# Optimization experiments

Hardware: AMD Instinct MI355X
Metric: run time of the kernel (lower is better)

The kernel has to match this reference:

```python
import jax, jax.numpy as jnp
import numpy as np

G, K = 60, 13  # SO(3) group size, neighbors per group element


def _gather(x, nei):
    # x: [N, C, G] -> [N, C, G, K] via fixed neighbor indices (len G*K)
    return x[:, :, nei].reshape(x.shape[0], x.shape[1], G, K)


def _comb(x, nei, W, b):
    # gather-then-(1,K)-Conv2d == contraction over (channel, neighbor)
    d = _gather(x, nei)                                   # [N,C,G,K]
    return jnp.einsum('ncgk,ock->nog', d, W) + b[None, :, None]


def setup_inputs() -> dict:
    key = jax.random.key(0)
    ks = jax.random.split(key, 8)
    N = 512
    feats = jax.random.normal(ks[0], (N, 32, G), jnp.float32)
    nei = jax.random.randint(ks[1], (G * K,), 0, G, jnp.int32)

    def w(k, o, c):
        return jax.random.normal(k, (o, c, K), jnp.float32) * (1.0 / np.sqrt(c * K))

    return {
        'feats': feats, 'nei': nei,
        'W_in': w(ks[2], 256, 32), 'b_in': jnp.zeros((256,), jnp.float32),
        'W_r1': w(ks[3], 512, 256), 'b_r1': jnp.zeros((512,), jnp.float32),
        'W_r2': w(ks[4], 256, 512), 'b_r2': jnp.zeros((256,), jnp.float32),
        'W_out': w(ks[5], 32, 256), 'b_out': jnp.zeros((32,), jnp.float32),
    }


def reference(feats, nei, W_in, b_in, W_r1, b_r1, W_r2, b_r2, W_out, b_out):
    # Conv_in: gather + (1,13) conv, 32 -> 256
    h = _comb(feats, nei, W_in, b_in)                      # [N,256,G]
    # Residual_Comb_Conv(256, 512, 256)
    r = jax.nn.relu(_comb(h, nei, W_r1, b_r1))             # [N,512,G]
    h = h + _comb(r, nei, W_r2, b_r2)                      # [N,256,G]
    # Conv_out: gather + (1,13) conv, 256 -> 32, then outer residual
    feats_eqv = _comb(h, nei, W_out, b_out) + feats        # [N,32,G]
    feats_inv = jnp.mean(feats_eqv, axis=-1)               # [N,32]
    feats_eqv = feats_eqv / jnp.maximum(
        jnp.linalg.norm(feats_eqv, axis=1, keepdims=True), 1e-4)
    feats_inv = feats_inv / jnp.maximum(
        jnp.linalg.norm(feats_inv, axis=1, keepdims=True), 1e-4)
    return feats_inv, feats_eqv
```

## Files before the change

kernel.cpp:

```cpp
#include <hip/hip_runtime.h>
#include <stdint.h>

#define GSZ 60
#define KNB 13
#define NPT 512

typedef __attribute__((ext_vector_type(4))) float f32x4;
typedef __attribute__((ext_vector_type(8))) short s16x8;

__device__ __forceinline__ ushort f2bf(float f) {
  union { float f; unsigned u; } v; v.f = f;
  unsigned r = v.u + 0x7fffu + ((v.u >> 16) & 1u);
  return (ushort)(r >> 16);
}
__device__ __forceinline__ float bf2f(ushort h) {
  union { unsigned u; float f; } v; v.u = ((unsigned)h) << 16;
  return v.f;
}

__device__ __forceinline__ void gload_lds16(const void* gsrc, void* ldst) {
  __builtin_amdgcn_global_load_lds(
      (const __attribute__((address_space(1))) uint32_t*)gsrc,
      (__attribute__((address_space(3))) uint32_t*)ldst, 16, 0, 0);
}

template <int N>
__device__ __forceinline__ void vwaitN() {
  if constexpr (N == 0) asm volatile("s_waitcnt vmcnt(0)" ::: "memory");
  else if constexpr (N == 3) asm volatile("s_waitcnt vmcnt(3)" ::: "memory");
  else if constexpr (N == 4) asm volatile("s_waitcnt vmcnt(4)" ::: "memory");
  else if constexpr (N == 6) asm volatile("s_waitcnt vmcnt(6)" ::: "memory");
  else asm volatile("s_waitcnt vmcnt(8)" ::: "memory");
}

__global__ __launch_bounds__(256) void prep_feats_k(const float* __restrict__ feats,
                                                    ushort* __restrict__ X0) {
  int idx = blockIdx.x * 256 + threadIdx.x;
  if (idx >= 61 * NPT * 32) return;
  int c = idx & 31;
  int t = idx >> 5;
  int n = t % NPT;
  int g = t / NPT;
  X0[idx] = (g < GSZ) ? f2bf(feats[(n * 32 + c) * GSZ + g]) : (ushort)0;
}

__global__ __launch_bounds__(256) void prep_wb_k(const float* __restrict__ W,
                                                 ushort* __restrict__ Wb,
                                                 int O, int OPAD, int C, int KPAD) {
  int idx = blockIdx.x * 256 + threadIdx.x;
  if (idx >= OPAD * KPAD) return;
  int o = idx / KPAD;
  int kk = idx - o * KPAD;
  int k = kk / C;
  int c = kk - k * C;
  Wb[idx] = (o < O && k < KNB) ? f2bf(W[(o * C + c) * KNB + k]) : (ushort)0;
}

template <int CIN, int KTOT, int OPAD, int OREAL, int BN, int MODE, bool RELU>
__global__ __launch_bounds__(256) void comb_gemm(
    const ushort* __restrict__ Xin, const ushort* __restrict__ Wb,
    const float* __restrict__ bias, const int* __restrict__ nei,
    ushort* __restrict__ Xout, float* __restrict__ Eq,
    const float* __restrict__ feats, int qb, int qe) {
  constexpr int BM = 128;
  constexpr int BK = 64;
  constexpr int TO = OPAD / BN;
  constexpr int TN = NPT / BM;
  constexpr int WN = BN / 2;
  constexpr int N_REP = WN / 16;
  constexpr int M_REP = 4;
  constexpr int CSH = (CIN == 32) ? 5 : (CIN == 256) ? 8 : 9;
  static_assert(CIN == (1 << CSH), "CIN pow2");

  __shared__ ushort smA[2][BM * BK];
  __shared__ ushort smB[2][BN * BK];
  __shared__ int nei_sh[16];

  const int nwg = TO * TN * GSZ;
  const int cpx = nwg >> 3;
  const int bid = blockIdx.x;
  const int idx = (bid & 7) * cpx + (bid >> 3);
  const int g = idx / (TO * TN);
  const int rem = idx - g * (TO * TN);
  const int nt = rem / TO;
  const int ot = rem - nt * TO;
  const int n0 = nt * BM;
  const int o0 = ot * BN;

  const int t = threadIdx.x;
  if (t < 14) nei_sh[t] = (t < KNB) ? nei[g * KNB + t] : GSZ;
  __syncthreads();

  const int w = t >> 6;
  const int l = t & 63;
  const int lrow = l & 15;
  const int lkg = l >> 4;
  const int wr = w >> 1;
  const int wc = w & 1;
  const int srow_w = w * 8;
  const int sr = l >> 3;
  const int slot = l & 7;

  int laneA[BM / 32], laneB[BN / 32], swz[BM / 32];
#pragma unroll
  for (int j = 0; j < BM / 32; ++j) {
    const int r = j * 32 + srow_w + sr;
    swz[j] = (slot ^ (r & 7)) << 3;
    laneA[j] = ((n0 + r) << CSH) + swz[j];
  }
#pragma unroll
  for (int j = 0; j < BN / 32; ++j) {
    const int r = j * 32 + srow_w + sr;
    laneB[j] = (o0 + r) * KTOT + ((slot ^ (r & 7)) << 3);
  }

  auto stage = [&](int buf, int q) {
    const int c0 = q * BK;
    if constexpr (CIN >= 64) {
      const int pbase = nei_sh[c0 >> CSH] * (NPT << CSH) + (c0 & (CIN - 1));
#pragma unroll
      for (int j = 0; j < BM / 32; ++j)
        gload_lds16(Xin + pbase + laneA[j], &smA[buf][(j * 32 + srow_w) * BK]);
    } else {
#pragma unroll
      for (int j = 0; j < BM / 32; ++j) {
        const int r = j * 32 + srow_w + sr;
        const int kk = c0 + swz[j];
        const int nbr = kk >> CSH;
        const int cc = kk & (CIN - 1);
        gload_lds16(Xin + ((nei_sh[nbr] * NPT + n0 + r) << CSH) + cc,
                    &smA[buf][(j * 32 + srow_w) * BK]);
      }
    }
#pragma unroll
    for (int j = 0; j < BN / 32; ++j)
      gload_lds16(Wb + laneB[j] + c0, &smB[buf][(j * 32 + srow_w) * BK]);
  };

  f32x4 acc[M_REP][N_REP] = {};

  stage(0, qb);
  asm volatile("s_waitcnt vmcnt(0)" ::: "memory");
  __builtin_amdgcn_s_barrier();

  int cur = 0;
#pragma unroll 1
  for (int q = qb; q < qe; ++q) {
    if (q + 1 < qe) stage(cur ^ 1, q + 1);
#pragma unroll
    for (int ks = 0; ks < 2; ++ks) {
      const int cb = ks * 4 + lkg;
      s16x8 bf[N_REP];
#pragma unroll
      for (int n = 0; n < N_REP; ++n) {
        const int r = wc * WN + n * 16 + lrow;
        bf[n] = *(const s16x8*)&smB[cur][r * BK + ((cb ^ (r & 7)) << 3)];
      }
#pragma unroll
      for (int m = 0; m < M_REP; ++m) {
        const int r = wr * 64 + m * 16 + lrow;
        s16x8 af = *(const s16x8*)&smA[cur][r * BK + ((cb ^ (r & 7)) << 3)];
#pragma unroll
        for (int n = 0; n < N_REP; ++n)
          acc[m][n] = __builtin_amdgcn_mfma_f32_16x16x32_bf16(af, bf[n], acc[m][n], 0, 0, 0);
      }
    }
    asm volatile("s_waitcnt vmcnt(0)" ::: "memory");
    __builtin_amdgcn_s_barrier();
    cur ^= 1;
  }

#pragma unroll
  for (int m = 0; m < M_REP; ++m) {
#pragma unroll
    for (int n = 0; n < N_REP; ++n) {
      const int oc = o0 + wc * WN + n * 16 + lrow;
      float bv;
      if (MODE == 2)
        bv = (oc < OREAL && feats) ? bias[oc] : 0.f;
      else
        bv = bias[oc];
#pragma unroll
      for (int r = 0; r < 4; ++r) {
        const int row = n0 + wr * 64 + m * 16 + lkg * 4 + r;
        float v = acc[m][n][r] + bv;
        if (MODE == 0) {
          if (RELU) v = v > 0.f ? v : 0.f;
          Xout[((size_t)g * NPT + row) * OPAD + oc] = f2bf(v);
        } else if (MODE == 1) {
          const size_t ix = ((size_t)g * NPT + row) * OPAD + oc;
          Xout[ix] = f2bf(bf2f(Xout[ix]) + v);
        } else {
          const float add = (oc < OREAL && feats) ? feats[((size_t)row * 32 + oc) * GSZ + g] : 0.f;
          Eq[((size_t)g * NPT + row) * 64 + oc] = v + add;
        }
      }
    }
  }
}

template <int CIN, int KTOT, int OPAD, int BM, int MODE, bool RELU>
__global__ __launch_bounds__(512) void comb8p(
    const ushort* __restrict__ Xin, const ushort* __restrict__ Wb,
    const float* __restrict__ bias, const int* __restrict__ nei,
    ushort* __restrict__ Xout) {
  constexpr int NT = KTOT / 64;
  constexpr int TN = NPT / BM;
  constexpr int TO = OPAD / 256;
  constexpr int WM = BM / 2;
  constexpr int M_REP = WM / 16;
  constexpr int MH = M_REP / 2;
  constexpr int LA = BM / 128;
  constexpr int LB = 2;
  constexpr int WS = 2 * (LA + LB);
  constexpr int WT = LA + LB;
  constexpr int CSH = (CIN == 256) ? 8 : 9;
  static_assert(CIN == (1 << CSH), "CIN pow2");

  __shared__ ushort smA[2][2][BM * 32];
  __shared__ ushort smB[2][2][256 * 32];
  __shared__ int nei_sh[16];

  const int nwg = TO * TN * GSZ;
  const int cpx = nwg >> 3;
  const int bid = blockIdx.x;
  const int idx = (bid & 7) * cpx + (bid >> 3);
  const int g = idx / (TO * TN);
  const int rem = idx - g * (TO * TN);
  const int nt = rem / TO;
  const int ot = rem - nt * TO;
  const int n0 = nt * BM;
  const int o0 = ot * 256;

  const int t = threadIdx.x;
  if (t < 14) nei_sh[t] = (t < KNB) ? nei[g * KNB + t] : GSZ;
  __syncthreads();

  const int w = t >> 6;
  const int l = t & 63;
  const int lrow = l & 15;
  const int lkg = l >> 4;
  const int wr = w >> 2;
  const int wc = w & 3;

  int laneA[LA], laneB[LB];
#pragma unroll
  for (int j = 0; j < LA; ++j) {
    const int r = w * (16 * LA) + j * 16 + (l >> 2);
    const int s = (l & 3) ^ ((r >> 1) & 3);
    laneA[j] = ((n0 + r) << CSH) + s * 8;
  }
#pragma unroll
  for (int j = 0; j < LB; ++j) {
    const int r = w * 32 + j * 16 + (l >> 2);
    const int s = (l & 3) ^ ((r >> 1) & 3);
    laneB[j] = (o0 + r) * KTOT + s * 8;
  }

  auto stageA = [&](int buf, int h, int tt) {
    const int k0 = tt * 64;
    const int pbase = nei_sh[k0 >> CSH] * (NPT << CSH) + (k0 & (CIN - 1)) + h * 32;
#pragma unroll
    for (int j = 0; j < LA; ++j)
      gload_lds16(Xin + pbase + laneA[j], &smA[buf][h][(w * (16 * LA) + j * 16) * 32]);
  };
  auto stageB = [&](int buf, int h, int tt) {
    const int kb = tt * 64 + h * 32;
#pragma unroll
    for (int j = 0; j < LB; ++j)
      gload_lds16(Wb + kb + laneB[j], &smB[buf][h][(w * 32 + j * 16) * 32]);
  };

  auto ridx = [&](int r) { return r * 32 + ((lkg ^ ((r >> 1) & 3)) << 3); };

  f32x4 acc[M_REP][4] = {};
  s16x8 bfr[4], afr[MH];

  stageA(0, 0, 0); stageB(0, 0, 0);
  stageA(0, 1, 0); stageB(0, 1, 0);
  if (NT > 1) { stageA(1, 0, 1); stageB(1, 0, 1); }
  vwaitN<WS>();
  __builtin_amdgcn_s_barrier();

#pragma unroll 1
  for (int tt = 0; tt < NT; ++tt) {
    const int buf = tt & 1;
#pragma unroll
    for (int n = 0; n < 4; ++n) bfr[n] = *(const s16x8*)&smB[buf][0][ridx(wc * 64 + n * 16 + lrow)];
#pragma unroll
    for (int m = 0; m < MH; ++m) afr[m] = *(const s16x8*)&smA[buf][0][ridx(wr * WM + m * 16 + lrow)];
    if (tt + 1 < NT) stageA(buf ^ 1, 1, tt + 1);
    __builtin_amdgcn_s_barrier();
    __builtin_amdgcn_s_setprio(1);
#pragma unroll
    for (int m = 0; m < MH; ++m)
#pragma unroll
      for (int n = 0; n < 4; ++n)
        acc[m][n] = __builtin_amdgcn_mfma_f32_16x16x32_bf16(afr[m], bfr[n], acc[m][n], 0, 0, 0);
    __builtin_amdgcn_s_setprio(0);
    __builtin_amdgcn_s_barrier();
#pragma unroll
    for (int m = 0; m < MH; ++m) afr[m] = *(const s16x8*)&smA[buf][0][ridx(wr * WM + (MH + m) * 16 + lrow)];
    if (tt + 1 < NT) stageB(buf ^ 1, 1, tt + 1);
    __builtin_amdgcn_s_barrier();
    __builtin_amdgcn_s_setprio(1);
#pragma unroll
    for (int m = 0; m < MH; ++m)
#pragma unroll
      for (int n = 0; n < 4; ++n)
        acc[MH + m][n] = __builtin_amdgcn_mfma_f32_16x16x32_bf16(afr[m], bfr[n], acc[MH + m][n], 0, 0, 0);
    __builtin_amdgcn_s_setprio(0);
    if (tt + 1 < NT) vwaitN<WS>(); else vwaitN<0>();
    __builtin_amdgcn_s_barrier();
#pragma unroll
    for (int n = 0; n < 4; ++n) bfr[n] = *(const s16x8*)&smB[buf][1][ridx(wc * 64 + n * 16 + lrow)];
#pragma unroll
    for (int m = 0; m < MH; ++m) afr[m] = *(const s16x8*)&smA[buf][1][ridx(wr * WM + m * 16 + lrow)];
    if (tt + 2 < NT) stageA(buf, 0, tt + 2);
    __builtin_amdgcn_s_barrier();
    __builtin_amdgcn_s_setprio(1);
#pragma unroll
    for (int m = 0; m < MH; ++m)
#pragma unroll
      for (int n = 0; n < 4; ++n)
        acc[m][n] = __builtin_amdgcn_mfma_f32_16x16x32_bf16(afr[m], bfr[n], acc[m][n], 0, 0, 0);
    __builtin_amdgcn_s_setprio(0);
    __builtin_amdgcn_s_barrier();
#pragma unroll
    for (int m = 0; m < MH; ++m) afr[m] = *(const s16x8*)&smA[buf][1][ridx(wr * WM + (MH + m) * 16 + lrow)];
    if (tt + 2 < NT) stageB(buf, 0, tt + 2);
    __builtin_amdgcn_s_barrier();
    __builtin_amdgcn_s_setprio(1);
#pragma unroll
    for (int m = 0; m < MH; ++m)
#pragma unroll
      for (int n = 0; n < 4; ++n)
        acc[MH + m][n] = __builtin_amdgcn_mfma_f32_16x16x32_bf16(afr[m], bfr[n], acc[MH + m][n], 0, 0, 0);
    __builtin_amdgcn_s_setprio(0);
    if (tt + 2 < NT) vwaitN<WS>();
    else if (tt + 1 < NT) vwaitN<WT>();
    else vwaitN<0>();
    __builtin_amdgcn_s_barrier();
  }

#pragma unroll
  for (int m = 0; m < M_REP; ++m) {
#pragma unroll
    for (int n = 0; n < 4; ++n) {
      const int oc = o0 + wc * 64 + n * 16 + lrow;
      const float bv = bias[oc];
#pragma unroll
      for (int r = 0; r < 4; ++r) {
        const int row = n0 + wr * WM + m * 16 + lkg * 4 + r;
        float v = acc[m][n][r] + bv;
        if (MODE == 0) {
          if (RELU) v = v > 0.f ? v : 0.f;
          Xout[((size_t)g * NPT + row) * OPAD + oc] = f2bf(v);
        } else {
          const size_t ix = ((size_t)g * NPT + row) * OPAD + oc;
          Xout[ix] = f2bf(bf2f(Xout[ix]) + v);
        }
      }
    }
  }
}

__global__ __launch_bounds__(256) void finalize_k(const float* __restrict__ Eq,
                                                  float* __restrict__ out) {
  const int n = blockIdx.x;
  const int t = threadIdx.x;
  const int c = t & 31;
  const int gs = t >> 5;
  constexpr size_t PART = (size_t)GSZ * NPT * 64;

  float invp = 0.f;
  for (int g = gs; g < GSZ; g += 8) {
    const size_t base = ((size_t)g * NPT + n) * 64 + c;
    float x = Eq[base] + Eq[PART + base] + Eq[2 * PART + base] + Eq[3 * PART + base];
    invp += x;
    float ss = x * x;
#pragma unroll
    for (int m = 16; m >= 1; m >>= 1) ss += __shfl_xor(ss, m, 64);
    float nrm = sqrtf(ss);
    nrm = nrm > 1e-4f ? nrm : 1e-4f;
    out[16384 + ((size_t)n * 32 + c) * GSZ + g] = x / nrm;
  }

  __shared__ float tmp[8][32];
  tmp[gs][c] = invp;
  __syncthreads();
  if (t < 32) {
    float s = 0.f;
#pragma unroll
    for (int i = 0; i < 8; ++i) s += tmp[i][t];
    s *= (1.f / 60.f);
    float ss = s * s;
#pragma unroll
    for (int m = 16; m >= 1; m >>= 1) ss += __shfl_xor(ss, m, 64);
    float nrm = sqrtf(ss);
    nrm = nrm > 1e-4f ? nrm : 1e-4f;
    out[(size_t)n * 32 + t] = s / nrm;
  }
}

extern "C" void kernel_launch(void* const* d_in, const int* in_sizes, int n_in,
                              void* d_out, int out_size, void* d_ws, size_t ws_size,
                              hipStream_t stream) {
  const float* feats = (const float*)d_in[0];
  const int* nei = (const int*)d_in[1];
  const float* W_in = (const float*)d_in[2];
  const float* b_in = (const float*)d_in[3];
  const float* W_r1 = (const float*)d_in[4];
  const float* b_r1 = (const float*)d_in[5];
  const float* W_r2 = (const float*)d_in[6];
  const float* b_r2 = (const float*)d_in[7];
  const float* W_out = (const float*)d_in[8];
  const float* b_out = (const float*)d_in[9];
  float* out = (float*)d_out;

  char* ws = (char*)d_ws;
  size_t off = 0;
  auto alloc = [&](size_t bytes) {
    void* p = ws + off;
    off += (bytes + 255) & ~(size_t)255;
    return p;
  };
  ushort* X0 = (ushort*)alloc((size_t)61 * NPT * 32 * 2);
  ushort* H1 = (ushort*)alloc((size_t)GSZ * NPT * 256 * 2);
  ushort* R = (ushort*)alloc((size_t)GSZ * NPT * 512 * 2);
  ushort* Wb_in = (ushort*)alloc((size_t)256 * 448 * 2);
  ushort* Wb_r1 = (ushort*)alloc((size_t)512 * 3328 * 2);
  ushort* Wb_r2 = (ushort*)alloc((size_t)256 * 6656 * 2);
  ushort* Wb_out = (ushort*)alloc((size_t)64 * 3328 * 2);
  float* Eq4 = (float*)R;

  prep_feats_k<<<(61 * NPT * 32 + 255) / 256, 256, 0, stream>>>(feats, X0);
  prep_wb_k<<<(256 * 448 + 255) / 256, 256, 0, stream>>>(W_in, Wb_in, 256, 256, 32, 448);
  prep_wb_k<<<(512 * 3328 + 255) / 256, 256, 0, stream>>>(W_r1, Wb_r1, 512, 512, 256, 3328);
  prep_wb_k<<<(256 * 6656 + 255) / 256, 256, 0, stream>>>(W_r2, Wb_r2, 256, 256, 512, 6656);
  prep_wb_k<<<(64 * 3328 + 255) / 256, 256, 0, stream>>>(W_out, Wb_out, 32, 64, 256, 3328);

  comb_gemm<32, 448, 256, 256, 128, 0, false><<<dim3(2 * 4 * GSZ), dim3(256), 0, stream>>>(
      X0, Wb_in, b_in, nei, H1, nullptr, nullptr, 0, 7);
  comb8p<256, 3328, 512, 256, 0, true><<<dim3(240), dim3(512), 0, stream>>>(
      H1, Wb_r1, b_r1, nei, R);
  comb8p<512, 6656, 256, 128, 1, false><<<dim3(240), dim3(512), 0, stream>>>(
      R, Wb_r2, b_r2, nei, H1);
  for (int kp = 0; kp < 4; ++kp) {
    comb_gemm<256, 3328, 64, 32, 64, 2, false><<<dim3(1 * 4 * GSZ), dim3(256), 0, stream>>>(
        H1, Wb_out, b_out, nei, nullptr, Eq4 + (size_t)kp * GSZ * NPT * 64,
        kp == 0 ? feats : nullptr, kp * 13, (kp + 1) * 13);
  }
  finalize_k<<<NPT, 256, 0, stream>>>(Eq4, out);
}
```

Baseline: 388.4 us.

## Use 256x256 tiles with split-K for the second residual conv plus combine kernel

The 512->256 residual conv previously used 128-row tiles over the full K of 6656. It now uses 256x256 tiles and splits K in two, keeping the same 240-block grid. Each split writes bf16 partials to a new workspace buffer. A separate vectorized combine kernel then adds both partials, the bias and the residual into H1. The larger tile is meant to improve operand reuse per MFMA. The cost is extra memory traffic for the partials, an additional kernel launch, and an extra bf16 rounding of the partial sums.

```diff
diff --git a/kernel.cpp b/kernel.cpp
--- a/kernel.cpp
+++ b/kernel.cpp
@@ -7,6 +7,7 @@
 
 typedef __attribute__((ext_vector_type(4))) float f32x4;
 typedef __attribute__((ext_vector_type(8))) short s16x8;
+typedef __attribute__((ext_vector_type(8))) ushort u16x8;
 
 __device__ __forceinline__ ushort f2bf(float f) {
   union { float f; unsigned u; } v; v.f = f;
@@ -22,15 +23,6 @@
   __builtin_amdgcn_global_load_lds(
       (const __attribute__((address_space(1))) uint32_t*)gsrc,
       (__attribute__((address_space(3))) uint32_t*)ldst, 16, 0, 0);
-}
-
-template <int N>
-__device__ __forceinline__ void vwaitN() {
-  if constexpr (N == 0) asm volatile("s_waitcnt vmcnt(0)" ::: "memory");
-  else if constexpr (N == 3) asm volatile("s_waitcnt vmcnt(3)" ::: "memory");
-  else if constexpr (N == 4) asm volatile("s_waitcnt vmcnt(4)" ::: "memory");
-  else if constexpr (N == 6) asm volatile("s_waitcnt vmcnt(6)" ::: "memory");
-  else asm volatile("s_waitcnt vmcnt(8)" ::: "memory");
 }
 
 __global__ __launch_bounds__(256) void prep_feats_k(const float* __restrict__ feats,
@@ -199,38 +191,36 @@
   }
 }
 
-template <int CIN, int KTOT, int OPAD, int BM, int MODE, bool RELU>
-__global__ __launch_bounds__(512) void comb8p(
+template <int CIN, int KTOT, int OPAD, int MODE, bool RELU, int SPLITK>
+__global__ __launch_bounds__(512, 2) void comb8p256(
     const ushort* __restrict__ Xin, const ushort* __restrict__ Wb,
     const float* __restrict__ bias, const int* __restrict__ nei,
     ushort* __restrict__ Xout) {
-  constexpr int NT = KTOT / 64;
+  constexpr int BM = 256, BN = 256;
+  constexpr int NTL = KTOT / 64 / SPLITK;
+  constexpr int TO = OPAD / BN;
   constexpr int TN = NPT / BM;
-  constexpr int TO = OPAD / 256;
-  constexpr int WM = BM / 2;
-  constexpr int M_REP = WM / 16;
-  constexpr int MH = M_REP / 2;
-  constexpr int LA = BM / 128;
-  constexpr int LB = 2;
-  constexpr int WS = 2 * (LA + LB);
-  constexpr int WT = LA + LB;
   constexpr int CSH = (CIN == 256) ? 8 : 9;
   static_assert(CIN == (1 << CSH), "CIN pow2");
 
   __shared__ ushort smA[2][2][BM * 32];
-  __shared__ ushort smB[2][2][256 * 32];
+  __shared__ ushort smB[2][2][BN * 32];
   __shared__ int nei_sh[16];
 
-  const int nwg = TO * TN * GSZ;
+  const int nparts = TO * TN * GSZ;
+  const int nwg = nparts * SPLITK;
   const int cpx = nwg >> 3;
   const int bid = blockIdx.x;
-  const int idx = (bid & 7) * cpx + (bid >> 3);
-  const int g = idx / (TO * TN);
-  const int rem = idx - g * (TO * TN);
+  const int idxa = (bid & 7) * cpx + (bid >> 3);
+  const int kp = idxa / nparts;
+  const int sub = idxa - kp * nparts;
+  const int g = sub / (TO * TN);
+  const int rem = sub - g * (TO * TN);
   const int nt = rem / TO;
   const int ot = rem - nt * TO;
   const int n0 = nt * BM;
-  const int o0 = ot * 256;
+  const int o0 = ot * BN;
+  const int qb = kp * NTL;
 
   const int t = threadIdx.x;
   if (t < 14) nei_sh[t] = (t < KNB) ? nei[g * KNB + t] : GSZ;
@@ -243,126 +233,143 @@
   const int wr = w >> 2;
   const int wc = w & 3;
 
-  int laneA[LA], laneB[LB];
-#pragma unroll
-  for (int j = 0; j < LA; ++j) {
-    const int r = w * (16 * LA) + j * 16 + (l >> 2);
+  int laneA[2], laneB[2];
+#pragma unroll
+  for (int j = 0; j < 2; ++j) {
+    const int r = w * 32 + j * 16 + (l >> 2);
     const int s = (l & 3) ^ ((r >> 1) & 3);
     laneA[j] = ((n0 + r) << CSH) + s * 8;
-  }
-#pragma unroll
-  for (int j = 0; j < LB; ++j) {
-    const int r = w * 32 + j * 16 + (l >> 2);
-    const int s = (l & 3) ^ ((r >> 1) & 3);
     laneB[j] = (o0 + r) * KTOT + s * 8;
   }
 
-  auto stageA = [&](int buf, int h, int tt) {
-    const int k0 = tt * 64;
-    const int pbase = nei_sh[k0 >> CSH] * (NPT << CSH) + (k0 & (CIN - 1)) + h * 32;
-#pragma unroll
-    for (int j = 0; j < LA; ++j)
-      gload_lds16(Xin + pbase + laneA[j], &smA[buf][h][(w * (16 * LA) + j * 16) * 32]);
+  auto stageA = [&](int buf, int h, int tg) {
+    const int k0 = tg * 64 + h * 32;
+    const int pbase = nei_sh[k0 >> CSH] * (NPT << CSH) + (k0 & (CIN - 1));
+#pragma unroll
+    for (int j = 0; j < 2; ++j)
+      gload_lds16(Xin + pbase + laneA[j], &smA[buf][h][(w * 32 + j * 16) * 32]);
   };
-  auto stageB = [&](int buf, int h, int tt) {
-    const int kb = tt * 64 + h * 32;
-#pragma unroll
-    for (int j = 0; j < LB; ++j)
+  auto stageB = [&](int buf, int h, int tg) {
+    const int kb = tg * 64 + h * 32;
+#pragma unroll
+    for (int j = 0; j < 2; ++j)
       gload_lds16(Wb + kb + laneB[j], &smB[buf][h][(w * 32 + j * 16) * 32]);
   };
 
   auto ridx = [&](int r) { return r * 32 + ((lkg ^ ((r >> 1) & 3)) << 3); };
 
-  f32x4 acc[M_REP][4] = {};
-  s16x8 bfr[4], afr[MH];
-
-  stageA(0, 0, 0); stageB(0, 0, 0);
-  stageA(0, 1, 0); stageB(0, 1, 0);
-  if (NT > 1) { stageA(1, 0, 1); stageB(1, 0, 1); }
-  vwaitN<WS>();
+  f32x4 acc[8][4] = {};
+  s16x8 bfr[4], afr[4];
+
+  stageA(0, 0, qb); stageB(0, 0, qb);
+  stageA(0, 1, qb); stageB(0, 1, qb);
+  stageA(1, 0, qb + 1); stageB(1, 0, qb + 1);
+  asm volatile("s_waitcnt vmcnt(8)" ::: "memory");
   __builtin_amdgcn_s_barrier();
 
 #pragma unroll 1
-  for (int tt = 0; tt < NT; ++tt) {
+  for (int tt = 0; tt < NTL; ++tt) {
     const int buf = tt & 1;
-#pragma unroll
-    for (int n = 0; n < 4; ++n) bfr[n] = *(const s16x8*)&smB[buf][0][ridx(wc * 64 + n * 16 + lrow)];
-#pragma unroll
-    for (int m = 0; m < MH; ++m) afr[m] = *(const s16x8*)&smA[buf][0][ridx(wr * WM + m * 16 + lrow)];
-    if (tt + 1 < NT) stageA(buf ^ 1, 1, tt + 1);
+    const int tg = qb + tt;
+#pragma unroll
+    for (int n = 0; n < 4; ++n)
+      bfr[n] = *(const s16x8*)&smB[buf][0][ridx(wc * 64 + n * 16 + lrow)];
+#pragma unroll
+    for (int m = 0; m < 4; ++m)
+      afr[m] = *(const s16x8*)&smA[buf][0][ridx(wr * 128 + m * 16 + lrow)];
+    if (tt + 1 < NTL) stageA(buf ^ 1, 1, tg + 1);
     __builtin_amdgcn_s_barrier();
     __builtin_amdgcn_s_setprio(1);
 #pragma unroll
-    for (int m = 0; m < MH; ++m)
+    for (int m = 0; m < 4; ++m)
 #pragma unroll
       for (int n = 0; n < 4; ++n)
         acc[m][n] = __builtin_amdgcn_mfma_f32_16x16x32_bf16(afr[m], bfr[n], acc[m][n], 0, 0, 0);
     __builtin_amdgcn_s_setprio(0);
     __builtin_amdgcn_s_barrier();
 #pragma unroll
-    for (int m = 0; m < MH; ++m) afr[m] = *(const s16x8*)&smA[buf][0][ridx(wr * WM + (MH + m) * 16 + lrow)];
-    if (tt + 1 < NT) stageB(buf ^ 1, 1, tt + 1);
+    for (int m = 0; m < 4; ++m)
+      afr[m] = *(const s16x8*)&smA[buf][0][ridx(wr * 128 + (4 + m) * 16 + lrow)];
+    if (tt + 1 < NTL) stageB(buf ^ 1, 1, tg + 1);
     __builtin_amdgcn_s_barrier();
     __builtin_amdgcn_s_setprio(1);
 #pragma unroll
-    for (int m = 0; m < MH; ++m)
+    for (int m = 0; m < 4; ++m)
 #pragma unroll
       for (int n = 0; n < 4; ++n)
-        acc[MH + m][n] = __builtin_amdgcn_mfma_f32_16x16x32_bf16(afr[m], bfr[n], acc[MH + m][n], 0, 0, 0);
+        acc[4 + m][n] = __builtin_amdgcn_mfma_f32_16x16x32_bf16(afr[m], bfr[n], acc[4 + m][n], 0, 0, 0);
     __builtin_amdgcn_s_setprio(0);
-    if (tt + 1 < NT) vwaitN<WS>(); else vwaitN<0>();
-    __builtin_amdgcn_s_barrier();
-#pragma unroll
-    for (int n = 0; n < 4; ++n) bfr[n] = *(const s16x8*)&smB[buf][1][ridx(wc * 64 + n * 16 + lrow)];
-#pragma unroll
-    for (int m = 0; m < MH; ++m) afr[m] = *(const s16x8*)&smA[buf][1][ridx(wr * WM + m * 16 + lrow)];
-    if (tt + 2 < NT) stageA(buf, 0, tt + 2);
+    if (tt + 1 < NTL) asm volatile("s_waitcnt vmcnt(8)" ::: "memory");
+    else asm volatile("s_waitcnt vmcnt(0)" ::: "memory");
+    __builtin_amdgcn_s_barrier();
+#pragma unroll
+    for (int n = 0; n < 4; ++n)
+      bfr[n] = *(const s16x8*)&smB[buf][1][ridx(wc * 64 + n * 16 + lrow)];
+#pragma unroll
+    for (int m = 0; m < 4; ++m)
+      afr[m] = *(const s16x8*)&smA[buf][1][ridx(wr * 128 + m * 16 + lrow)];
+    if (tt + 2 < NTL) stageA(buf, 0, tg + 2);
     __builtin_amdgcn_s_barrier();
     __builtin_amdgcn_s_setprio(1);
 #pragma unroll
-    for (int m = 0; m < MH; ++m)
+    for (int m = 0; m < 4; ++m)
 #pragma unroll
       for (int n = 0; n < 4; ++n)
         acc[m][n] = __builtin_amdgcn_mfma_f32_16x16x32_bf16(afr[m], bfr[n], acc[m][n], 0, 0, 0);
     __builtin_amdgcn_s_setprio(0);
     __builtin_amdgcn_s_barrier();
 #pragma unroll
-    for (int m = 0; m < MH; ++m) afr[m] = *(const s16x8*)&smA[buf][1][ridx(wr * WM + (MH + m) * 16 + lrow)];
-    if (tt + 2 < NT) stageB(buf, 0, tt + 2);
+    for (int m = 0; m < 4; ++m)
+      afr[m] = *(const s16x8*)&smA[buf][1][ridx(wr * 128 + (4 + m) * 16 + lrow)];
+    if (tt + 2 < NTL) stageB(buf, 0, tg + 2);
     __builtin_amdgcn_s_barrier();
     __builtin_amdgcn_s_setprio(1);
 #pragma unroll
-    for (int m = 0; m < MH; ++m)
+    for (int m = 0; m < 4; ++m)
 #pragma unroll
       for (int n = 0; n < 4; ++n)
-        acc[MH + m][n] = __builtin_amdgcn_mfma_f32_16x16x32_bf16(afr[m], bfr[n], acc[MH + m][n], 0, 0, 0);
+        acc[4 + m][n] = __builtin_amdgcn_mfma_f32_16x16x32_bf16(afr[m], bfr[n], acc[4 + m][n], 0, 0, 0);
     __builtin_amdgcn_s_setprio(0);
-    if (tt + 2 < NT) vwaitN<WS>();
-    else if (tt + 1 < NT) vwaitN<WT>();
-    else vwaitN<0>();
-    __builtin_amdgcn_s_barrier();
-  }
-
-#pragma unroll
-  for (int m = 0; m < M_REP; ++m) {
+    if (tt + 2 < NTL) asm volatile("s_waitcnt vmcnt(8)" ::: "memory");
+    else if (tt + 1 < NTL) asm volatile("s_waitcnt vmcnt(4)" ::: "memory");
+    else asm volatile("s_waitcnt vmcnt(0)" ::: "memory");
+    __builtin_amdgcn_s_barrier();
+  }
+
+  ushort* outp = Xout;
+  if constexpr (MODE == 3) outp += (size_t)kp * GSZ * NPT * OPAD;
+#pragma unroll
+  for (int m = 0; m < 8; ++m) {
 #pragma unroll
     for (int n = 0; n < 4; ++n) {
       const int oc = o0 + wc * 64 + n * 16 + lrow;
-      const float bv = bias[oc];
+      const float bv = (MODE == 0) ? bias[oc] : 0.f;
 #pragma unroll
       for (int r = 0; r < 4; ++r) {
-        const int row = n0 + wr * WM + m * 16 + lkg * 4 + r;
+        const int row = n0 + wr * 128 + m * 16 + lkg * 4 + r;
         float v = acc[m][n][r] + bv;
-        if (MODE == 0) {
-          if (RELU) v = v > 0.f ? v : 0.f;
-          Xout[((size_t)g * NPT + row) * OPAD + oc] = f2bf(v);
-        } else {
-          const size_t ix = ((size_t)g * NPT + row) * OPAD + oc;
-          Xout[ix] = f2bf(bf2f(Xout[ix]) + v);
-        }
+        if (MODE == 0 && RELU) v = v > 0.f ? v : 0.f;
+        outp[((size_t)g * NPT + row) * OPAD + oc] = f2bf(v);
       }
     }
   }
+}
+
+__global__ __launch_bounds__(256) void combine_k(ushort* __restrict__ H1,
+                                                 const ushort* __restrict__ PK,
+                                                 const float* __restrict__ bias) {
+  constexpr size_t TOT = (size_t)GSZ * NPT * 256;
+  const size_t i = ((size_t)blockIdx.x * 256 + threadIdx.x) * 8;
+  if (i >= TOT) return;
+  const int oc = (int)(i & 255);
+  u16x8 h = *(const u16x8*)&H1[i];
+  u16x8 p0 = *(const u16x8*)&PK[i];
+  u16x8 p1 = *(const u16x8*)&PK[TOT + i];
+  u16x8 o;
+#pragma unroll
+  for (int j = 0; j < 8; ++j)
+    o[j] = f2bf(bf2f(h[j]) + bf2f(p0[j]) + bf2f(p1[j]) + bias[oc + j]);
+  *(u16x8*)&H1[i] = o;
 }
 
 __global__ __launch_bounds__(256) void finalize_k(const float* __restrict__ Eq,
@@ -428,6 +435,7 @@
   ushort* X0 = (ushort*)alloc((size_t)61 * NPT * 32 * 2);
   ushort* H1 = (ushort*)alloc((size_t)GSZ * NPT * 256 * 2);
   ushort* R = (ushort*)alloc((size_t)GSZ * NPT * 512 * 2);
+  ushort* PK = (ushort*)alloc((size_t)2 * GSZ * NPT * 256 * 2);
   ushort* Wb_in = (ushort*)alloc((size_t)256 * 448 * 2);
   ushort* Wb_r1 = (ushort*)alloc((size_t)512 * 3328 * 2);
   ushort* Wb_r2 = (ushort*)alloc((size_t)256 * 6656 * 2);
@@ -442,10 +450,11 @@
 
   comb_gemm<32, 448, 256, 256, 128, 0, false><<<dim3(2 * 4 * GSZ), dim3(256), 0, stream>>>(
       X0, Wb_in, b_in, nei, H1, nullptr, nullptr, 0, 7);
-  comb8p<256, 3328, 512, 256, 0, true><<<dim3(240), dim3(512), 0, stream>>>(
+  comb8p256<256, 3328, 512, 0, true, 1><<<dim3(240), dim3(512), 0, stream>>>(
       H1, Wb_r1, b_r1, nei, R);
-  comb8p<512, 6656, 256, 128, 1, false><<<dim3(240), dim3(512), 0, stream>>>(
-      R, Wb_r2, b_r2, nei, H1);
+  comb8p256<512, 6656, 256, 3, false, 2><<<dim3(240), dim3(512), 0, stream>>>(
+      R, Wb_r2, b_r2, nei, PK);
+  combine_k<<<dim3((GSZ * NPT * 256 / 8 + 255) / 256), dim3(256), 0, stream>>>(H1, PK, b_r2);
   for (int kp = 0; kp < 4; ++kp) {
     comb_gemm<256, 3328, 64, 32, 64, 2, false><<<dim3(1 * 4 * GSZ), dim3(256), 0, stream>>>(
         H1, Wb_out, b_out, nei, nullptr, Eq4 + (size_t)kp * GSZ * NPT * 64,
```

After: 361.3 us. 7.0% less time.
